# Kernel optimization log

Measured on AMD Instinct MI355X. Metric: run time of the kernel, lower is better.

## Reference

```python
import jax, jax.numpy as jnp
import numpy as np

N_NODES = 100000
N_EDGES = 1600000
D_IN = 64
D_HID = 64
D_OUT = 64


def setup_inputs() -> dict:
    key = jax.random.key(0)
    ks = jax.random.split(key, 12)
    x = jax.random.normal(ks[0], (N_NODES, D_IN), dtype=jnp.float32)
    edge_index = jax.random.randint(ks[1], (2, N_EDGES), 0, N_NODES, dtype=jnp.int64)
    def lin(k, fan_in, fan_out):
        s = 1.0 / np.sqrt(fan_in)
        return jax.random.uniform(k, (fan_out, fan_in), jnp.float32, -s, s)
    dims = [(D_IN, D_HID), (D_HID, D_HID), (D_HID, D_OUT)]
    params = {}
    for i, (di, do) in enumerate(dims):
        params[f"W_l{i}"] = lin(ks[2 + 3 * i], di, do)      # weight for aggregated neighbors
        params[f"W_r{i}"] = lin(ks[3 + 3 * i], di, do)      # weight for root/self features
        params[f"b{i}"] = jnp.zeros((do,), jnp.float32)
    return {"x": x, "edge_index": edge_index, **params}


def _sage_conv(x, src, dst, W_l, W_r, b):
    # mean aggregation of source features at destination nodes
    agg = jax.ops.segment_sum(x[src], dst, num_segments=N_NODES)          # [N, d]
    cnt = jax.ops.segment_sum(jnp.ones_like(dst, dtype=x.dtype), dst, num_segments=N_NODES)
    mean = agg / jnp.maximum(cnt, 1.0)[:, None]
    return mean @ W_l.T + x @ W_r.T + b


def reference(x, edge_index, W_l0, W_r0, b0, W_l1, W_r1, b1, W_l2, W_r2, b2):
    src, dst = edge_index[0], edge_index[1]
    h = jax.nn.relu(_sage_conv(x, src, dst, W_l0, W_r0, b0))
    h = jax.nn.relu(_sage_conv(h, src, dst, W_l1, W_r1, b1))
    out = _sage_conv(h, src, dst, W_l2, W_r2, b2)
    return out
```

## Files before the change

### kernel.cpp

```cpp
#include <hip/hip_runtime.h>

#define N_NODES 100000
#define N_EDGES 1600000
#define D 64
#define NB 131
#define NBUCKETS 764
#define PCHUNK 8192
#define NCHUNK 196
#define PBLK 1024

typedef unsigned int u32;
typedef unsigned short u16;
typedef _Float16 f16;
typedef f16 f16x8 __attribute__((ext_vector_type(8)));
typedef float f32x4 __attribute__((ext_vector_type(4)));

__global__ __launch_bounds__(PBLK) void hist_kernel(const int* __restrict__ dst,
                                                    int* __restrict__ hist) {
    __shared__ int hcnt[NBUCKETS];
    int t = threadIdx.x;
    int c0 = blockIdx.x * PCHUNK;
    int nloc = min(PCHUNK, N_EDGES - c0);
    for (int i = t; i < NBUCKETS; i += PBLK) hcnt[i] = 0;
    __syncthreads();
    for (int i = t; i < nloc; i += PBLK) atomicAdd(&hcnt[dst[c0 + i] / NB], 1);
    __syncthreads();
    for (int i = t; i < NBUCKETS; i += PBLK) hist[blockIdx.x * NBUCKETS + i] = hcnt[i];
}

__global__ __launch_bounds__(1024) void cscan_kernel(int* __restrict__ hist,
                                                     int* __restrict__ bptr) {
    __shared__ int s[1024];
    int t = threadIdx.x;
    int tot = 0;
    if (t < NBUCKETS)
        for (int c = 0; c < NCHUNK; ++c) tot += hist[c * NBUCKETS + t];
    s[t] = tot;
    __syncthreads();
    for (int off = 1; off < 1024; off <<= 1) {
        int a = (t >= off) ? s[t - off] : 0;
        __syncthreads();
        s[t] += a;
        __syncthreads();
    }
    if (t < NBUCKETS) {
        int run = s[t] - tot;
        bptr[t] = run;
        for (int c = 0; c < NCHUNK; ++c) {
            int v = hist[c * NBUCKETS + t];
            hist[c * NBUCKETS + t] = run;
            run += v;
        }
    }
    if (t == NBUCKETS - 1) bptr[NBUCKETS] = s[t];
}

__global__ __launch_bounds__(PBLK) void part_kernel(const int* __restrict__ src,
                                                    const int* __restrict__ dst,
                                                    const int* __restrict__ cbase,
                                                    u32* __restrict__ pairs) {
    __shared__ int hcur[NBUCKETS];
    __shared__ int hb[NBUCKETS];
    int t = threadIdx.x;
    int c0 = blockIdx.x * PCHUNK;
    int nloc = min(PCHUNK, N_EDGES - c0);
    for (int i = t; i < NBUCKETS; i += PBLK) {
        hcur[i] = 0;
        hb[i] = cbase[blockIdx.x * NBUCKETS + i];
    }
    __syncthreads();
    for (int i = t; i < nloc; i += PBLK) {
        int s = src[c0 + i];
        int d = dst[c0 + i];
        int b = d / NB;
        int r = atomicAdd(&hcur[b], 1);
        pairs[hb[b] + r] = ((u32)(d - b * NB) << 24) | (u32)s;
    }
}

__global__ __launch_bounds__(256) void local_csr_kernel(
    const u32* __restrict__ pairs, const int* __restrict__ bptr,
    int* __restrict__ row_ptr, int* __restrict__ cnt, float* __restrict__ inv,
    int* __restrict__ csr_src)
{
    __shared__ int lcnt[NB];
    __shared__ int lofs[NB];
    __shared__ int s[256];

    int t = threadIdx.x, b = blockIdx.x;
    int e0 = bptr[b], e1 = bptr[b + 1];
    int nb0 = b * NB;

    for (int i = t; i < NB; i += 256) lcnt[i] = 0;
    __syncthreads();
    for (int e = e0 + t; e < e1; e += 256) atomicAdd(&lcnt[pairs[e] >> 24], 1);
    __syncthreads();

    int v = (t < NB) ? lcnt[t] : 0;
    s[t] = v;
    __syncthreads();
    for (int off = 1; off < 256; off <<= 1) {
        int a = (t >= off) ? s[t - off] : 0;
        __syncthreads();
        s[t] += a;
        __syncthreads();
    }
    if (t < NB) {
        int node = nb0 + t;
        if (node < N_NODES) {
            int excl = s[t] - v;
            lofs[t] = excl;
            row_ptr[node] = e0 + excl;
            cnt[node] = v;
            inv[node] = 1.0f / fmaxf((float)v, 1.0f);
        }
        lcnt[t] = 0;
    }
    __syncthreads();
    for (int e = e0 + t; e < e1; e += 256) {
        u32 p = pairs[e];
        int dl = (int)(p >> 24);
        int pos = atomicAdd(&lcnt[dl], 1);
        csr_src[e0 + lofs[dl] + pos] = (int)(p & 0xFFFFFFu);
    }
}

__global__ void tof16_kernel(const float* __restrict__ in, u16* __restrict__ outh, int n4) {
    int i = blockIdx.x * blockDim.x + threadIdx.x;
    if (i < n4) {
        float4 v = reinterpret_cast<const float4*>(in)[i];
        union { f16 h[4]; uint2 u; } cv;
        cv.h[0] = (f16)v.x; cv.h[1] = (f16)v.y; cv.h[2] = (f16)v.z; cv.h[3] = (f16)v.w;
        reinterpret_cast<uint2*>(outh)[i] = cv.u;
    }
}

__global__ void prep_bfrag(const float* __restrict__ Wl0, const float* __restrict__ Wr0,
                           const float* __restrict__ Wl1, const float* __restrict__ Wr1,
                           const float* __restrict__ Wl2, const float* __restrict__ Wr2,
                           uint4* __restrict__ Bfrag) {
    int idx = blockIdx.x * blockDim.x + threadIdx.x;
    if (idx >= 3 * 16 * 64) return;
    int layer = idx >> 10, r = idx & 1023, f = r >> 6, l = r & 63;
    const float* Wl = layer == 0 ? Wl0 : layer == 1 ? Wl1 : Wl2;
    const float* Wr = layer == 0 ? Wr0 : layer == 1 ? Wr1 : Wr2;
    int ktg = f >> 2, nt = f & 3;
    const float* W = (ktg & 2) ? Wr : Wl;
    int o = nt * 16 + (l & 15);
    int k = (ktg & 1) * 32 + (l >> 4) * 8;
    const float* s = W + o * 64 + k;
    float4 v0 = *reinterpret_cast<const float4*>(s);
    float4 v1 = *reinterpret_cast<const float4*>(s + 4);
    union { f16x8 h; uint4 u; } cv;
    cv.h[0] = (f16)v0.x; cv.h[1] = (f16)v0.y; cv.h[2] = (f16)v0.z; cv.h[3] = (f16)v0.w;
    cv.h[4] = (f16)v1.x; cv.h[5] = (f16)v1.y; cv.h[6] = (f16)v1.z; cv.h[7] = (f16)v1.w;
    Bfrag[idx] = cv.u;
}

__device__ __forceinline__ void add8(float* va, uint4 r) {
    union { uint4 u; f16x8 h; } cv; cv.u = r;
    #pragma unroll
    for (int e = 0; e < 8; ++e) va[e] += (float)cv.h[e];
}

__global__ __launch_bounds__(256, 8) void sage_layer(
    const u16* __restrict__ hh,
    const int* __restrict__ row_ptr, const int* __restrict__ cnt,
    const int* __restrict__ csr_src, const float* __restrict__ inv,
    const uint4* __restrict__ Bfrag,
    const float* __restrict__ bvec,
    float* __restrict__ outf,
    u16* __restrict__ outh,
    int relu)
{
    __shared__ u16 Atile[4][16][128];

    int t = threadIdx.x;
    int w    = t >> 6;
    int lane = t & 63;
    int j8   = lane & 7;
    int sg   = lane >> 3;
    const uint4* rows = reinterpret_cast<const uint4*>(hh);

    int base = blockIdx.x * 64 + w * 16;

    float bias[4];
    #pragma unroll
    for (int nt = 0; nt < 4; ++nt) bias[nt] = bvec[nt * 16 + (lane & 15)];

    #pragma unroll
    for (int slot = 0; slot < 2; ++slot) {
        int n = slot * 8 + sg;
        int node = base + n;
        bool valid = node < N_NODES;
        int nodec = valid ? node : N_NODES - 1;
        uint4 selfrow = rows[nodec * 8 + j8];
        int s0 = row_ptr[nodec];
        int c  = valid ? cnt[nodec] : 0;
        float va[8] = {0.f,0.f,0.f,0.f,0.f,0.f,0.f,0.f};
        int j = 0;
        int i0 = 0, i1 = 0, i2 = 0, i3 = 0;
        bool have = (c >= 4);
        if (have) {
            i0 = csr_src[s0];     i1 = csr_src[s0 + 1];
            i2 = csr_src[s0 + 2]; i3 = csr_src[s0 + 3];
        }
        while (have) {
            uint4 r0 = rows[i0 * 8 + j8];
            uint4 r1 = rows[i1 * 8 + j8];
            uint4 r2 = rows[i2 * 8 + j8];
            uint4 r3 = rows[i3 * 8 + j8];
            j += 4;
            have = (j + 4 <= c);
            if (have) {
                i0 = csr_src[s0 + j];     i1 = csr_src[s0 + j + 1];
                i2 = csr_src[s0 + j + 2]; i3 = csr_src[s0 + j + 3];
            }
            add8(va, r0); add8(va, r1); add8(va, r2); add8(va, r3);
        }
        for (; j < c; ++j) {
            add8(va, rows[csr_src[s0 + j] * 8 + j8]);
        }
        float sc = inv[nodec];
        union { f16x8 h; uint4 u; } mv;
        #pragma unroll
        for (int e = 0; e < 8; ++e) mv.h[e] = (f16)(va[e] * sc);
        int chunk = j8 ^ (n & 7);
        if (valid) {
            *reinterpret_cast<uint4*>(&Atile[w][n][chunk * 8]) = mv.u;
            *reinterpret_cast<uint4*>(&Atile[w][n][64 + chunk * 8]) = selfrow;
        }
    }

    f32x4 acc[4] = {};
    int row = lane & 15, kg = lane >> 4;
    #pragma unroll
    for (int ktg = 0; ktg < 4; ++ktg) {
        int idx16 = ktg * 4 + kg;
        int swz = (idx16 & 8) | ((idx16 & 7) ^ (row & 7));
        uint4 a = *reinterpret_cast<const uint4*>(&Atile[w][row][swz * 8]);
        union { uint4 u; f16x8 h; } av; av.u = a;
        #pragma unroll
        for (int nt = 0; nt < 4; ++nt) {
            union { uint4 u; f16x8 h; } bv; bv.u = Bfrag[(ktg * 4 + nt) * 64 + lane];
            acc[nt] = __builtin_amdgcn_mfma_f32_16x16x32_f16(av.h, bv.h, acc[nt], 0, 0, 0);
        }
    }

    #pragma unroll
    for (int nt = 0; nt < 4; ++nt) {
        int o = nt * 16 + (lane & 15);
        #pragma unroll
        for (int r = 0; r < 4; ++r) {
            int n = kg * 4 + r;
            int node = base + n;
            if (node < N_NODES) {
                float vout = acc[nt][r] + bias[nt];
                if (relu) vout = fmaxf(vout, 0.f);
                if (outf) outf[node * 64 + o] = vout;
                if (outh) {
                    union { f16 h; u16 u; } cv; cv.h = (f16)vout;
                    outh[node * 64 + o] = cv.u;
                }
            }
        }
    }
}

extern "C" void kernel_launch(void* const* d_in, const int* in_sizes, int n_in,
                              void* d_out, int out_size, void* d_ws, size_t ws_size,
                              hipStream_t stream) {
    const float* x   = (const float*)d_in[0];
    const int*   ei  = (const int*)d_in[1];
    const int*   src = ei;
    const int*   dst = ei + N_EDGES;
    const float* Wl0 = (const float*)d_in[2];
    const float* Wr0 = (const float*)d_in[3];
    const float* b0  = (const float*)d_in[4];
    const float* Wl1 = (const float*)d_in[5];
    const float* Wr1 = (const float*)d_in[6];
    const float* b1  = (const float*)d_in[7];
    const float* Wl2 = (const float*)d_in[8];
    const float* Wr2 = (const float*)d_in[9];
    const float* b2  = (const float*)d_in[10];
    float* out = (float*)d_out;

    char* p = (char*)d_ws;
    auto take = [&](size_t bytes) { char* r = p; p += (bytes + 255) & ~(size_t)255; return r; };
    int*   hist    = (int*)take((size_t)NCHUNK * NBUCKETS * 4);
    int*   bptr    = (int*)take((size_t)(NBUCKETS + 1) * 4);
    u32*   pairs   = (u32*)take((size_t)N_EDGES * 4);
    int*   csr_src = (int*)take((size_t)N_EDGES * 4);
    int*   row_ptr = (int*)take((size_t)N_NODES * 4);
    int*   cnt     = (int*)take((size_t)N_NODES * 4);
    float* inv     = (float*)take((size_t)N_NODES * 4);
    uint4* Bfrag   = (uint4*)take((size_t)3 * 16 * 64 * 16);
    u16*   xh      = (u16*)take((size_t)N_NODES * D * 2);
    u16*   h0h     = (u16*)take((size_t)N_NODES * D * 2);
    u16*   h1h     = (u16*)take((size_t)N_NODES * D * 2);

    const int BLK = 256;
    const int conv_grid  = (N_NODES * D / 4 + BLK - 1) / BLK;
    const int layer_grid = (N_NODES + 63) / 64;

    hist_kernel<<<NCHUNK, PBLK, 0, stream>>>(dst, hist);
    cscan_kernel<<<1, 1024, 0, stream>>>(hist, bptr);
    part_kernel<<<NCHUNK, PBLK, 0, stream>>>(src, dst, hist, pairs);
    local_csr_kernel<<<NBUCKETS, BLK, 0, stream>>>(pairs, bptr, row_ptr, cnt, inv, csr_src);
    tof16_kernel<<<conv_grid, BLK, 0, stream>>>(x, xh, N_NODES * D / 4);
    prep_bfrag<<<(3 * 1024 + BLK - 1) / BLK, BLK, 0, stream>>>(Wl0, Wr0, Wl1, Wr1, Wl2, Wr2, Bfrag);

    sage_layer<<<layer_grid, BLK, 0, stream>>>(xh,  row_ptr, cnt, csr_src, inv, Bfrag,        b0, nullptr, h0h, 1);
    sage_layer<<<layer_grid, BLK, 0, stream>>>(h0h, row_ptr, cnt, csr_src, inv, Bfrag + 1024, b1, nullptr, h1h, 1);
    sage_layer<<<layer_grid, BLK, 0, stream>>>(h1h, row_ptr, cnt, csr_src, inv, Bfrag + 2048, b2, out, nullptr, 0);
}
```

Baseline: 182.8 us.

## Split bucket scan into multi-block kernels and unroll neighbor gather by eight

The single-block cumulative scan is split into three kernels: a column sum over chunks spread across several blocks, a 1024-thread scan over bucket totals, and a multi-block rebase that writes per-chunk offsets. The aim is to remove a serial single-block bottleneck on the critical path, at the cost of two extra kernel launches. The gather loop in the SAGE layer now issues eight index loads and eight row loads per iteration instead of a software-pipelined four, to keep more memory requests in flight. The occupancy hint is lowered from 8 to 6 waves to leave room for the extra registers.

```diff
diff --git a/kernel.cpp b/kernel.cpp
--- a/kernel.cpp
+++ b/kernel.cpp
@@ -28,14 +28,21 @@
     for (int i = t; i < NBUCKETS; i += PBLK) hist[blockIdx.x * NBUCKETS + i] = hcnt[i];
 }
 
-__global__ __launch_bounds__(1024) void cscan_kernel(int* __restrict__ hist,
+__global__ void colsum_kernel(const int* __restrict__ hist, int* __restrict__ btot) {
+    int t = blockIdx.x * blockDim.x + threadIdx.x;
+    if (t < NBUCKETS) {
+        int s = 0;
+        for (int c = 0; c < NCHUNK; ++c) s += hist[c * NBUCKETS + t];
+        btot[t] = s;
+    }
+}
+
+__global__ __launch_bounds__(1024) void bscan_kernel(const int* __restrict__ btot,
                                                      int* __restrict__ bptr) {
     __shared__ int s[1024];
     int t = threadIdx.x;
-    int tot = 0;
-    if (t < NBUCKETS)
-        for (int c = 0; c < NCHUNK; ++c) tot += hist[c * NBUCKETS + t];
-    s[t] = tot;
+    int v = (t < NBUCKETS) ? btot[t] : 0;
+    s[t] = v;
     __syncthreads();
     for (int off = 1; off < 1024; off <<= 1) {
         int a = (t >= off) ? s[t - off] : 0;
@@ -43,16 +50,20 @@
         s[t] += a;
         __syncthreads();
     }
+    if (t < NBUCKETS) bptr[t] = s[t] - v;
+    if (t == NBUCKETS - 1) bptr[NBUCKETS] = s[t];
+}
+
+__global__ void rebase_kernel(int* __restrict__ hist, const int* __restrict__ bptr) {
+    int t = blockIdx.x * blockDim.x + threadIdx.x;
     if (t < NBUCKETS) {
-        int run = s[t] - tot;
-        bptr[t] = run;
+        int run = bptr[t];
         for (int c = 0; c < NCHUNK; ++c) {
             int v = hist[c * NBUCKETS + t];
             hist[c * NBUCKETS + t] = run;
             run += v;
         }
     }
-    if (t == NBUCKETS - 1) bptr[NBUCKETS] = s[t];
 }
 
 __global__ __launch_bounds__(PBLK) void part_kernel(const int* __restrict__ src,
@@ -163,7 +174,7 @@
     for (int e = 0; e < 8; ++e) va[e] += (float)cv.h[e];
 }
 
-__global__ __launch_bounds__(256, 8) void sage_layer(
+__global__ __launch_bounds__(256, 6) void sage_layer(
     const u16* __restrict__ hh,
     const int* __restrict__ row_ptr, const int* __restrict__ cnt,
     const int* __restrict__ csr_src, const float* __restrict__ inv,
@@ -199,24 +210,25 @@
         int c  = valid ? cnt[nodec] : 0;
         float va[8] = {0.f,0.f,0.f,0.f,0.f,0.f,0.f,0.f};
         int j = 0;
-        int i0 = 0, i1 = 0, i2 = 0, i3 = 0;
-        bool have = (c >= 4);
-        if (have) {
-            i0 = csr_src[s0];     i1 = csr_src[s0 + 1];
-            i2 = csr_src[s0 + 2]; i3 = csr_src[s0 + 3];
-        }
-        while (have) {
-            uint4 r0 = rows[i0 * 8 + j8];
-            uint4 r1 = rows[i1 * 8 + j8];
-            uint4 r2 = rows[i2 * 8 + j8];
-            uint4 r3 = rows[i3 * 8 + j8];
+        for (; j + 8 <= c; j += 8) {
+            int i0 = csr_src[s0 + j];     int i1 = csr_src[s0 + j + 1];
+            int i2 = csr_src[s0 + j + 2]; int i3 = csr_src[s0 + j + 3];
+            int i4 = csr_src[s0 + j + 4]; int i5 = csr_src[s0 + j + 5];
+            int i6 = csr_src[s0 + j + 6]; int i7 = csr_src[s0 + j + 7];
+            uint4 r0 = rows[i0 * 8 + j8]; uint4 r1 = rows[i1 * 8 + j8];
+            uint4 r2 = rows[i2 * 8 + j8]; uint4 r3 = rows[i3 * 8 + j8];
+            uint4 r4 = rows[i4 * 8 + j8]; uint4 r5 = rows[i5 * 8 + j8];
+            uint4 r6 = rows[i6 * 8 + j8]; uint4 r7 = rows[i7 * 8 + j8];
+            add8(va, r0); add8(va, r1); add8(va, r2); add8(va, r3);
+            add8(va, r4); add8(va, r5); add8(va, r6); add8(va, r7);
+        }
+        if (j + 4 <= c) {
+            int i0 = csr_src[s0 + j];     int i1 = csr_src[s0 + j + 1];
+            int i2 = csr_src[s0 + j + 2]; int i3 = csr_src[s0 + j + 3];
+            uint4 r0 = rows[i0 * 8 + j8]; uint4 r1 = rows[i1 * 8 + j8];
+            uint4 r2 = rows[i2 * 8 + j8]; uint4 r3 = rows[i3 * 8 + j8];
+            add8(va, r0); add8(va, r1); add8(va, r2); add8(va, r3);
             j += 4;
-            have = (j + 4 <= c);
-            if (have) {
-                i0 = csr_src[s0 + j];     i1 = csr_src[s0 + j + 1];
-                i2 = csr_src[s0 + j + 2]; i3 = csr_src[s0 + j + 3];
-            }
-            add8(va, r0); add8(va, r1); add8(va, r2); add8(va, r3);
         }
         for (; j < c; ++j) {
             add8(va, rows[csr_src[s0 + j] * 8 + j8]);
@@ -288,6 +300,7 @@
     char* p = (char*)d_ws;
     auto take = [&](size_t bytes) { char* r = p; p += (bytes + 255) & ~(size_t)255; return r; };
     int*   hist    = (int*)take((size_t)NCHUNK * NBUCKETS * 4);
+    int*   btot    = (int*)take((size_t)NBUCKETS * 4);
     int*   bptr    = (int*)take((size_t)(NBUCKETS + 1) * 4);
     u32*   pairs   = (u32*)take((size_t)N_EDGES * 4);
     int*   csr_src = (int*)take((size_t)N_EDGES * 4);
@@ -302,9 +315,12 @@
     const int BLK = 256;
     const int conv_grid  = (N_NODES * D / 4 + BLK - 1) / BLK;
     const int layer_grid = (N_NODES + 63) / 64;
+    const int bgrid      = (NBUCKETS + BLK - 1) / BLK;
 
     hist_kernel<<<NCHUNK, PBLK, 0, stream>>>(dst, hist);
-    cscan_kernel<<<1, 1024, 0, stream>>>(hist, bptr);
+    colsum_kernel<<<bgrid, BLK, 0, stream>>>(hist, btot);
+    bscan_kernel<<<1, 1024, 0, stream>>>(btot, bptr);
+    rebase_kernel<<<bgrid, BLK, 0, stream>>>(hist, bptr);
     part_kernel<<<NCHUNK, PBLK, 0, stream>>>(src, dst, hist, pairs);
     local_csr_kernel<<<NBUCKETS, BLK, 0, stream>>>(pairs, bptr, row_ptr, cnt, inv, csr_src);
     tof16_kernel<<<conv_grid, BLK, 0, stream>>>(x, xh, N_NODES * D / 4);
```

Measured after the change: 208.1 us. +13.9%, slower.
